# Performance work log

Measured on AMD Instinct MI355X. Metric: run time of the kernel, lower is better.

The kernel has to match this reference:

```python
import jax, jax.numpy as jnp
import numpy as np

NTOKENS = 8192   # max_ntokens
TOPK = 2
H = 1024         # hidden
FFN = 4096       # ffn_hidden = 4*hidden
E = 8            # nexperts
M = NTOKENS * TOPK          # total dispatched rows (flux_m_max)
CAP = M // E                # balanced rows per expert


def setup_inputs() -> dict:
    key = jax.random.key(0)
    k1, k2, k3, k4 = jax.random.split(key, 4)
    x = jax.random.normal(k1, (NTOKENS, H), jnp.float32)
    weight0 = jax.random.normal(k2, (E, H, FFN), jnp.float32) * 0.02
    weight1 = jax.random.normal(k3, (E, FFN, H), jnp.float32) * 0.02
    # Balanced routing: scatter_index[t, k] is the row in the expert-sorted
    # dispatched buffer; a permutation of arange(M) gives exactly CAP rows/expert.
    scatter_index = jax.random.permutation(k4, M).reshape(NTOKENS, TOPK).astype(jnp.int32)
    splits = jnp.full((E,), CAP, dtype=jnp.int32)  # rows per expert, sum == M
    return {"x": x, "weight0": weight0, "weight1": weight1,
            "scatter_index": scatter_index, "splits": splits}


def reference(x, weight0, weight1, scatter_index, splits):
    ntokens, topk = scatter_index.shape
    n_exp, h, ffn = weight0.shape
    m = ntokens * topk
    cap = m // n_exp  # splits are balanced by construction (== splits[e])
    # --- AG-scatter: place each (token, k) replica at its dispatched row ---
    vals = jnp.repeat(x, topk, axis=0)                              # [M, h]
    dispatched = jnp.zeros((m, h), x.dtype).at[scatter_index.reshape(-1)].set(vals)
    xe = dispatched.reshape(n_exp, cap, h)                          # [E, C, h]
    # --- grouped GEMM 0 + exact GELU (torch F.gelu default = erf form) ---
    mid = jax.nn.gelu(jnp.einsum('ech,ehf->ecf', xe, weight0), approximate=False)
    # --- grouped GEMM 1 ---
    ye = jnp.einsum('ecf,efh->ech', mid, weight1).reshape(m, h)     # [M, h]
    # --- gather-RS: combine topk expert outputs per token ---
    return ye[scatter_index].sum(axis=1)                            # [ntokens, h]
```

## Files before the change

### kernel.cpp

```cpp
#include <hip/hip_runtime.h>
#include <hip/hip_bf16.h>
#include <cstdint>

constexpr int NT   = 8192;
constexpr int H    = 1024;
constexpr int FFN  = 4096;
constexpr int E    = 8;
constexpr int M    = NT * 2;
constexpr int CAP  = M / E;

typedef unsigned short u16;
typedef short short8 __attribute__((ext_vector_type(8)));
typedef float f32x4 __attribute__((ext_vector_type(4)));

__device__ __forceinline__ u16 f2bf(float f) {
  union { float f; unsigned u; } c{f};
  unsigned r = (c.u + 0x7FFFu + ((c.u >> 16) & 1u)) >> 16;
  return (u16)r;
}
__device__ __forceinline__ float bf2f(u16 u) {
  union { unsigned u; float f; } c{((unsigned)u) << 16};
  return c.f;
}
__device__ __forceinline__ void async16(const void* g, void* l) {
  auto gp = reinterpret_cast<const __attribute__((address_space(1))) unsigned*>(
      reinterpret_cast<uintptr_t>(g));
  auto lp = reinterpret_cast<__attribute__((address_space(3))) unsigned*>(
      reinterpret_cast<uintptr_t>(l));
  __builtin_amdgcn_global_load_lds(gp, lp, 16, 0, 0);
}

__device__ __forceinline__ float gelu_fast(float x) {
  const float u = x * x;
  const float w = x * (-2.30220795f + -0.102943895f * u);
  return x * __frcp_rn(1.0f + exp2f(w));
}

__device__ __forceinline__ void transpose_body(const float* __restrict__ W,
                                               u16* __restrict__ WT,
                                               int K, int N, int tb,
                                               float (*tile)[65]) {
  const int ntx = N >> 6;
  const int per = ntx * (K >> 6);
  const int e   = tb / per;
  const int rem = tb - e * per;
  const int bx  = rem % ntx;
  const int by  = rem / ntx;
  const float* Wp = W + (size_t)e * K * N;
  u16* Tp = WT + (size_t)e * K * N;
  const int k0 = by * 64, n0 = bx * 64;
  const int tid = threadIdx.x;

  const int u = tid & 15, krb = tid >> 4;
#pragma unroll
  for (int p = 0; p < 4; ++p) {
    const int kr = p * 16 + krb;
    float4 v = *(const float4*)&Wp[(size_t)(k0 + kr) * N + n0 + u * 4];
    tile[kr][u * 4 + 0] = v.x;
    tile[kr][u * 4 + 1] = v.y;
    tile[kr][u * 4 + 2] = v.z;
    tile[kr][u * 4 + 3] = v.w;
  }
  __syncthreads();

  const int n = tid >> 3, cb = tid & 7;
#pragma unroll
  for (int p = 0; p < 2; ++p) {
    const int nn = p * 32 + n;
    u16 pack[8];
#pragma unroll
    for (int j = 0; j < 8; ++j) pack[j] = f2bf(tile[cb * 8 + j][nn]);
    *(short8*)&Tp[(size_t)(n0 + nn) * K + k0 + cb * 8] = *(short8*)pack;
  }
}

__device__ __forceinline__ void scatter_body(const float* __restrict__ x,
                                             const int* __restrict__ sidx,
                                             u16* __restrict__ disp, int b) {
  const int tid = threadIdx.x;
  const int half = tid >> 7;
  const int r = tid & 127;
#pragma unroll
  for (int it = 0; it < 2; ++it) {
    const int t = it * 4096 + b * 2 + half;
    const int r0 = sidx[2 * t + 0];
    const int r1 = sidx[2 * t + 1];
    const float4* xr = (const float4*)(x + (size_t)t * H);
    float4 v0 = xr[r * 2 + 0];
    float4 v1 = xr[r * 2 + 1];
    u16 pk[8] = {f2bf(v0.x), f2bf(v0.y), f2bf(v0.z), f2bf(v0.w),
                 f2bf(v1.x), f2bf(v1.y), f2bf(v1.z), f2bf(v1.w)};
    *(short8*)&disp[(size_t)r0 * H + r * 8] = *(short8*)pk;
    *(short8*)&disp[(size_t)r1 * H + r * 8] = *(short8*)pk;
  }
}

__global__ __launch_bounds__(256)
void pre_kernel(const float* __restrict__ x, const float* __restrict__ w0,
                const float* __restrict__ w1, const int* __restrict__ sidx,
                u16* __restrict__ wt0, u16* __restrict__ wt1,
                u16* __restrict__ disp) {
  __shared__ float tile[64][65];
  const int b = blockIdx.x;
  if (b < 2048) { scatter_body(x, sidx, disp, b); return; }
  if (b < 10240) { transpose_body(w0, wt0, H, FFN, b - 2048, tile); return; }
  transpose_body(w1, wt1, FFN, H, b - 10240, tile);
}

__global__ __launch_bounds__(256)
void transpose_cvt_kernel(const float* __restrict__ W, u16* __restrict__ WT,
                          int K, int N) {
  __shared__ float tile[64][65];
  transpose_body(W, WT, K, N, blockIdx.x, tile);
}

template <bool GELU>
__global__ __launch_bounds__(256)
void gemm_bt_kernel(const u16* __restrict__ A,
                    const u16* __restrict__ Bt,
                    u16* __restrict__ C,
                    int Mn, int Nn, int Kn, int ny) {
  __shared__ __align__(16) u16 lA[128 * 64];
  __shared__ __align__(16) u16 lB[128 * 64];

  const int b = blockIdx.x;
  const int e = b & 7;
  const int t = b >> 3;
  const int q = t & 15, s = t >> 4;
  const int sy = ny >> 2;
  const int sm = s % sy, sn = s / sy;
  const int tm = sm * 4 + (q & 3), tn = sn * 4 + (q >> 2);
  const int m0 = tm * 128, n0 = tn * 128;

  const u16* Ae = A  + (size_t)e * Mn * Kn + (size_t)m0 * Kn;
  const u16* Be = Bt + (size_t)e * Nn * Kn + (size_t)n0 * Kn;
  u16* Ce = C + (size_t)e * Mn * Nn;

  const int tid  = threadIdx.x;
  const int lane = tid & 63;
  const int wave = tid >> 6;
  const int wr = wave >> 1, wc = wave & 1;
  const int lhi = lane >> 4, llo = lane & 15;

  const int sr = lane >> 3;
  const int gc = (lane & 7) ^ sr;

  f32x4 acc[4][4] = {};

  for (int kt = 0; kt < Kn; kt += 64) {
#pragma unroll
    for (int s2 = 0; s2 < 4; ++s2) {
      const int i = wave * 4 + s2;
      const int row = i * 8 + sr;
      async16(Ae + (size_t)row * Kn + kt + gc * 8, &lA[i * 512]);
      async16(Be + (size_t)row * Kn + kt + gc * 8, &lB[i * 512]);
    }
    __syncthreads();

#pragma unroll 1
    for (int ks = 0; ks < 2; ++ks) {
      short8 af[4], bf[4];
#pragma unroll
      for (int i = 0; i < 4; ++i) {
        const int row = wr * 64 + i * 16 + llo;
        const int pc = (ks * 4 + lhi) ^ (llo & 7);
        af[i] = *(const short8*)&lA[row * 64 + pc * 8];
      }
#pragma unroll
      for (int j = 0; j < 4; ++j) {
        const int row = wc * 64 + j * 16 + llo;
        const int pc = (ks * 4 + lhi) ^ (llo & 7);
        bf[j] = *(const short8*)&lB[row * 64 + pc * 8];
      }
#pragma unroll
      for (int i = 0; i < 4; ++i)
#pragma unroll
        for (int j = 0; j < 4; ++j)
          acc[i][j] = __builtin_amdgcn_mfma_f32_16x16x32_bf16(af[i], bf[j], acc[i][j], 0, 0, 0);
    }
    __syncthreads();
  }

#pragma unroll
  for (int i = 0; i < 4; ++i) {
    const int mrow = m0 + wr * 64 + i * 16 + lhi * 4;
#pragma unroll
    for (int j = 0; j < 4; ++j) {
      const int ncol = n0 + wc * 64 + j * 16 + llo;
#pragma unroll
      for (int r = 0; r < 4; ++r) {
        float v = acc[i][j][r];
        if (GELU) v = gelu_fast(v);
        Ce[(size_t)(mrow + r) * Nn + ncol] = f2bf(v);
      }
    }
  }
}

__global__ __launch_bounds__(256)
void gather_sum_kernel(const u16* __restrict__ ye,
                       const int* __restrict__ sidx,
                       float* __restrict__ out) {
  const int tid = threadIdx.x;
  const int half = tid >> 7;
  const int r = tid & 127;
#pragma unroll
  for (int it = 0; it < 2; ++it) {
    const int t = it * 4096 + blockIdx.x * 2 + half;
    const int r0 = sidx[2 * t + 0];
    const int r1 = sidx[2 * t + 1];
    short8 a = *(const short8*)&ye[(size_t)r0 * H + r * 8];
    short8 b = *(const short8*)&ye[(size_t)r1 * H + r * 8];
    float4 s0, s1;
    s0.x = bf2f((u16)a[0]) + bf2f((u16)b[0]);
    s0.y = bf2f((u16)a[1]) + bf2f((u16)b[1]);
    s0.z = bf2f((u16)a[2]) + bf2f((u16)b[2]);
    s0.w = bf2f((u16)a[3]) + bf2f((u16)b[3]);
    s1.x = bf2f((u16)a[4]) + bf2f((u16)b[4]);
    s1.y = bf2f((u16)a[5]) + bf2f((u16)b[5]);
    s1.z = bf2f((u16)a[6]) + bf2f((u16)b[6]);
    s1.w = bf2f((u16)a[7]) + bf2f((u16)b[7]);
    float4* orow = (float4*)(out + (size_t)t * H);
    orow[r * 2 + 0] = s0;
    orow[r * 2 + 1] = s1;
  }
}

extern "C" void kernel_launch(void* const* d_in, const int* in_sizes, int n_in,
                              void* d_out, int out_size, void* d_ws, size_t ws_size,
                              hipStream_t stream) {
  (void)in_sizes; (void)n_in; (void)out_size;
  const float* x    = (const float*)d_in[0];
  const float* w0   = (const float*)d_in[1];
  const float* w1   = (const float*)d_in[2];
  const int*   sidx = (const int*)d_in[3];
  float* out = (float*)d_out;

  char* ws = (char*)d_ws;
  const size_t MB = 1024ull * 1024;
  u16* wt0  = (u16*)ws;
  u16* wt1  = (u16*)(ws + 64 * MB);
  u16* disp = (u16*)(ws + 128 * MB);
  u16* mid  = (u16*)(ws + 160 * MB);
  u16* ye   = disp;
  const bool roomy = ws_size >= 288 * MB;

  if (roomy) {
    pre_kernel<<<18432, 256, 0, stream>>>(x, w0, w1, sidx, wt0, wt1, disp);
    gemm_bt_kernel<true><<<4096, 256, 0, stream>>>(disp, wt0, mid, CAP, FFN, H, CAP / 128);
    gemm_bt_kernel<false><<<1024, 256, 0, stream>>>(mid, wt1, ye, CAP, H, FFN, CAP / 128);
  } else {
    wt1 = wt0;
    pre_kernel<<<10240, 256, 0, stream>>>(x, w0, w1, sidx, wt0, wt1, disp);
    gemm_bt_kernel<true><<<4096, 256, 0, stream>>>(disp, wt0, mid, CAP, FFN, H, CAP / 128);
    transpose_cvt_kernel<<<8192, 256, 0, stream>>>(w1, wt1, FFN, H);
    gemm_bt_kernel<false><<<1024, 256, 0, stream>>>(mid, wt1, ye, CAP, H, FFN, CAP / 128);
  }
  gather_sum_kernel<<<2048, 256, 0, stream>>>(ye, sidx, out);
}
```

Baseline: 689.9 us.

## Read fp32 weights directly in GEMMs, dropping separate transpose-convert pass

Removes the weight transpose/bf16-convert pre-pass and instead has each GEMM block load fp32 weight tiles in their native [K,N] layout, converting to bf16 into a padded LDS tile. B fragments are then gathered with eight scalar 16-bit LDS reads per fragment. This avoids writing and rereading transposed weight copies, but every M-tile block now re-reads and re-converts the fp32 weights (twice the bytes of bf16). It also replaces the async LDS loads with synchronous loads and adds strided scalar LDS reads in the inner loop.

New measurement: 762.4 us. 10.5% more time.

```diff
diff --git a/kernel.cpp b/kernel.cpp
--- a/kernel.cpp
+++ b/kernel.cpp
@@ -13,6 +13,8 @@
 typedef short short8 __attribute__((ext_vector_type(8)));
 typedef float f32x4 __attribute__((ext_vector_type(4)));
 
+constexpr int BS = 130;
+
 __device__ __forceinline__ u16 f2bf(float f) {
   union { float f; unsigned u; } c{f};
   unsigned r = (c.u + 0x7FFFu + ((c.u >> 16) & 1u)) >> 16;
@@ -36,47 +38,10 @@
   return x * __frcp_rn(1.0f + exp2f(w));
 }
 
-__device__ __forceinline__ void transpose_body(const float* __restrict__ W,
-                                               u16* __restrict__ WT,
-                                               int K, int N, int tb,
-                                               float (*tile)[65]) {
-  const int ntx = N >> 6;
-  const int per = ntx * (K >> 6);
-  const int e   = tb / per;
-  const int rem = tb - e * per;
-  const int bx  = rem % ntx;
-  const int by  = rem / ntx;
-  const float* Wp = W + (size_t)e * K * N;
-  u16* Tp = WT + (size_t)e * K * N;
-  const int k0 = by * 64, n0 = bx * 64;
-  const int tid = threadIdx.x;
-
-  const int u = tid & 15, krb = tid >> 4;
-#pragma unroll
-  for (int p = 0; p < 4; ++p) {
-    const int kr = p * 16 + krb;
-    float4 v = *(const float4*)&Wp[(size_t)(k0 + kr) * N + n0 + u * 4];
-    tile[kr][u * 4 + 0] = v.x;
-    tile[kr][u * 4 + 1] = v.y;
-    tile[kr][u * 4 + 2] = v.z;
-    tile[kr][u * 4 + 3] = v.w;
-  }
-  __syncthreads();
-
-  const int n = tid >> 3, cb = tid & 7;
-#pragma unroll
-  for (int p = 0; p < 2; ++p) {
-    const int nn = p * 32 + n;
-    u16 pack[8];
-#pragma unroll
-    for (int j = 0; j < 8; ++j) pack[j] = f2bf(tile[cb * 8 + j][nn]);
-    *(short8*)&Tp[(size_t)(n0 + nn) * K + k0 + cb * 8] = *(short8*)pack;
-  }
-}
-
-__device__ __forceinline__ void scatter_body(const float* __restrict__ x,
-                                             const int* __restrict__ sidx,
-                                             u16* __restrict__ disp, int b) {
+__global__ __launch_bounds__(256)
+void scatter_kernel(const float* __restrict__ x, const int* __restrict__ sidx,
+                    u16* __restrict__ disp) {
+  const int b = blockIdx.x;
   const int tid = threadIdx.x;
   const int half = tid >> 7;
   const int r = tid & 127;
@@ -95,33 +60,14 @@
   }
 }
 
-__global__ __launch_bounds__(256)
-void pre_kernel(const float* __restrict__ x, const float* __restrict__ w0,
-                const float* __restrict__ w1, const int* __restrict__ sidx,
-                u16* __restrict__ wt0, u16* __restrict__ wt1,
-                u16* __restrict__ disp) {
-  __shared__ float tile[64][65];
-  const int b = blockIdx.x;
-  if (b < 2048) { scatter_body(x, sidx, disp, b); return; }
-  if (b < 10240) { transpose_body(w0, wt0, H, FFN, b - 2048, tile); return; }
-  transpose_body(w1, wt1, FFN, H, b - 10240, tile);
-}
-
-__global__ __launch_bounds__(256)
-void transpose_cvt_kernel(const float* __restrict__ W, u16* __restrict__ WT,
-                          int K, int N) {
-  __shared__ float tile[64][65];
-  transpose_body(W, WT, K, N, blockIdx.x, tile);
-}
-
 template <bool GELU>
 __global__ __launch_bounds__(256)
-void gemm_bt_kernel(const u16* __restrict__ A,
-                    const u16* __restrict__ Bt,
-                    u16* __restrict__ C,
-                    int Mn, int Nn, int Kn, int ny) {
+void gemm_native_kernel(const u16* __restrict__ A,
+                        const float* __restrict__ W,
+                        u16* __restrict__ C,
+                        int Mn, int Nn, int Kn, int ny) {
   __shared__ __align__(16) u16 lA[128 * 64];
-  __shared__ __align__(16) u16 lB[128 * 64];
+  __shared__ __align__(16) u16 lBT[64 * BS];
 
   const int b = blockIdx.x;
   const int e = b & 7;
@@ -132,8 +78,8 @@
   const int tm = sm * 4 + (q & 3), tn = sn * 4 + (q >> 2);
   const int m0 = tm * 128, n0 = tn * 128;
 
-  const u16* Ae = A  + (size_t)e * Mn * Kn + (size_t)m0 * Kn;
-  const u16* Be = Bt + (size_t)e * Nn * Kn + (size_t)n0 * Kn;
+  const u16*   Ae = A + (size_t)e * Mn * Kn + (size_t)m0 * Kn;
+  const float* We = W + (size_t)e * Kn * Nn + n0;
   u16* Ce = C + (size_t)e * Mn * Nn;
 
   const int tid  = threadIdx.x;
@@ -145,6 +91,9 @@
   const int sr = lane >> 3;
   const int gc = (lane & 7) ^ sr;
 
+  const int bo = tid & 15;
+  const int bk = tid >> 4;
+
   f32x4 acc[4][4] = {};
 
   for (int kt = 0; kt < Kn; kt += 64) {
@@ -153,7 +102,16 @@
       const int i = wave * 4 + s2;
       const int row = i * 8 + sr;
       async16(Ae + (size_t)row * Kn + kt + gc * 8, &lA[i * 512]);
-      async16(Be + (size_t)row * Kn + kt + gc * 8, &lB[i * 512]);
+    }
+#pragma unroll
+    for (int it = 0; it < 4; ++it) {
+      const int k = it * 16 + bk;
+      const float* src = We + (size_t)(kt + k) * Nn + bo * 8;
+      float4 v0 = *(const float4*)src;
+      float4 v1 = *(const float4*)(src + 4);
+      u16 pk[8] = {f2bf(v0.x), f2bf(v0.y), f2bf(v0.z), f2bf(v0.w),
+                   f2bf(v1.x), f2bf(v1.y), f2bf(v1.z), f2bf(v1.w)};
+      *(short8*)&lBT[k * BS + bo * 8] = *(short8*)pk;
     }
     __syncthreads();
 
@@ -168,9 +126,13 @@
       }
 #pragma unroll
       for (int j = 0; j < 4; ++j) {
-        const int row = wc * 64 + j * 16 + llo;
-        const int pc = (ks * 4 + lhi) ^ (llo & 7);
-        bf[j] = *(const short8*)&lB[row * 64 + pc * 8];
+        const int n = wc * 64 + j * 16 + llo;
+        const int kb = (ks * 4 + lhi) * 8;
+        u16 btmp[8];
+#pragma unroll
+        for (int j2 = 0; j2 < 8; ++j2)
+          btmp[j2] = lBT[(kb + j2) * BS + n];
+        bf[j] = *(short8*)btmp;
       }
 #pragma unroll
       for (int i = 0; i < 4; ++i)
@@ -229,7 +191,7 @@
 extern "C" void kernel_launch(void* const* d_in, const int* in_sizes, int n_in,
                               void* d_out, int out_size, void* d_ws, size_t ws_size,
                               hipStream_t stream) {
-  (void)in_sizes; (void)n_in; (void)out_size;
+  (void)in_sizes; (void)n_in; (void)out_size; (void)ws_size;
   const float* x    = (const float*)d_in[0];
   const float* w0   = (const float*)d_in[1];
   const float* w1   = (const float*)d_in[2];
@@ -238,23 +200,14 @@
 
   char* ws = (char*)d_ws;
   const size_t MB = 1024ull * 1024;
-  u16* wt0  = (u16*)ws;
-  u16* wt1  = (u16*)(ws + 64 * MB);
-  u16* disp = (u16*)(ws + 128 * MB);
-  u16* mid  = (u16*)(ws + 160 * MB);
+  u16* disp = (u16*)ws;
+  u16* mid  = (u16*)(ws + 64 * MB);
   u16* ye   = disp;
-  const bool roomy = ws_size >= 288 * MB;
-
-  if (roomy) {
-    pre_kernel<<<18432, 256, 0, stream>>>(x, w0, w1, sidx, wt0, wt1, disp);
-    gemm_bt_kernel<true><<<4096, 256, 0, stream>>>(disp, wt0, mid, CAP, FFN, H, CAP / 128);
-    gemm_bt_kernel<false><<<1024, 256, 0, stream>>>(mid, wt1, ye, CAP, H, FFN, CAP / 128);
-  } else {
-    wt1 = wt0;
-    pre_kernel<<<10240, 256, 0, stream>>>(x, w0, w1, sidx, wt0, wt1, disp);
-    gemm_bt_kernel<true><<<4096, 256, 0, stream>>>(disp, wt0, mid, CAP, FFN, H, CAP / 128);
-    transpose_cvt_kernel<<<8192, 256, 0, stream>>>(w1, wt1, FFN, H);
-    gemm_bt_kernel<false><<<1024, 256, 0, stream>>>(mid, wt1, ye, CAP, H, FFN, CAP / 128);
-  }
+
+  scatter_kernel<<<2048, 256, 0, stream>>>(x, sidx, disp);
+  gemm_native_kernel<true><<<4096, 256, 0, stream>>>(
+      disp, w0, mid, CAP, FFN, H, CAP / 128);
+  gemm_native_kernel<false><<<1024, 256, 0, stream>>>(
+      mid, w1, ye, CAP, H, FFN, CAP / 128);
   gather_sum_kernel<<<2048, 256, 0, stream>>>(ye, sidx, out);
 }
```
